# Performance work log

Hardware: AMD Instinct MI355X
Metric: run time of the kernel (lower is better)

The kernel has to match this reference:

```python
import jax, jax.numpy as jnp
import numpy as np

IOU_EPS = 1e-6  # eps from RotatedIoULoss init
LOSS_WEIGHT = 1.0


def cross2(a, b):
    return a[..., 0] * b[..., 1] - a[..., 1] * b[..., 0]


def box2corners(box):
    # box: (n,5) = (x, y, w, h, angle) -> corners (n,4,2), counter-clockwise
    x, y, w, h, a = (box[:, i] for i in range(5))
    tx = jnp.array([0.5, -0.5, -0.5, 0.5], dtype=box.dtype)
    ty = jnp.array([0.5, 0.5, -0.5, -0.5], dtype=box.dtype)
    cx = tx[None, :] * w[:, None]  # (n,4) local x
    cy = ty[None, :] * h[:, None]  # (n,4) local y
    cos, sin = jnp.cos(a)[:, None], jnp.sin(a)[:, None]
    rx = cx * cos - cy * sin + x[:, None]
    ry = cx * sin + cy * cos + y[:, None]
    return jnp.stack([rx, ry], axis=-1)


def box_intersection(c1, c2):
    # pairwise (aligned) edge-edge intersections: (n,4,4,2) points, (n,4,4) valid mask
    p1 = c1[:, :, None, :]                             # (n,4,1,2) edge starts of box1
    d1 = (jnp.roll(c1, -1, axis=1) - c1)[:, :, None, :]
    p2 = c2[:, None, :, :]                             # (n,1,4,2) edge starts of box2
    d2 = (jnp.roll(c2, -1, axis=1) - c2)[:, None, :, :]
    den = cross2(d1, d2)                               # (n,4,4)
    dp = p2 - p1
    safe = jnp.where(den == 0, 1.0, den)
    t = cross2(dp, d2) / safe
    u = cross2(dp, d1) / safe
    mask = (den != 0) & (t > 0) & (t < 1) & (u > 0) & (u < 1)
    pts = p1 + t[..., None] * d1
    return pts, mask


def box1_in_box2(c1, c2):
    # which corners of box1 lie strictly inside box2 (projection test, as in mmcv)
    a = c2[:, 0:1, :]
    b = c2[:, 1:2, :]
    d = c2[:, 3:4, :]
    ab, ad, am = b - a, d - a, c1 - a                  # (n,4,2)
    pab = jnp.sum(am * ab, -1)
    nab = jnp.sum(ab * ab, -1)
    pad = jnp.sum(am * ad, -1)
    nad = jnp.sum(ad * ad, -1)
    return (pab > 0) & (pab < nab) & (pad > 0) & (pad < nad)


def oriented_box_intersection_area(c1, c2):
    # convex intersection polygon area via vertex gathering + angular sort + shoelace
    inter_pts, inter_mask = box_intersection(c1, c2)
    m1 = box1_in_box2(c1, c2)                          # (n,4)
    m2 = box1_in_box2(c2, c1)                          # (n,4)
    n = c1.shape[0]
    verts = jnp.concatenate([c1, c2, inter_pts.reshape(n, 16, 2)], axis=1)  # (n,24,2)
    mask = jnp.concatenate([m1, m2, inter_mask.reshape(n, 16)], axis=1)     # (n,24)
    num = jnp.sum(mask, axis=1)                        # (n,) valid vertex count
    maskf = mask.astype(verts.dtype)[..., None]
    center = jnp.sum(verts * maskf, axis=1) / jnp.maximum(num, 1)[:, None].astype(verts.dtype)
    rel = verts - center[:, None, :]
    ang = jnp.arctan2(rel[..., 1], rel[..., 0])
    ang = jnp.where(mask, ang, 1e6)                    # invalid vertices sort last
    order = jnp.argsort(ang, axis=1)
    sv = jnp.take_along_axis(verts, order[..., None], axis=1)  # sorted CCW
    sm = jnp.take_along_axis(mask, order, axis=1)
    first = sv[:, 0:1, :]
    poly = jnp.where(sm[..., None], sv, first)         # pad with first vertex -> closed polygon
    nxt = jnp.roll(poly, -1, axis=1)
    area = 0.5 * jnp.abs(jnp.sum(cross2(poly, nxt), axis=1))
    return jnp.where(num >= 3, area, 0.0)


def diff_iou_rotated_2d(pred, target):
    c1 = box2corners(pred)
    c2 = box2corners(target)
    inter = oriented_box_intersection_area(c1, c2)
    a1 = pred[:, 2] * pred[:, 3]
    a2 = target[:, 2] * target[:, 3]
    return inter / (a1 + a2 - inter)


def setup_inputs() -> dict:
    key = jax.random.key(0)
    n = 1_000_000
    k1, k2, k3, k4, k5, k6 = jax.random.split(key, 6)
    xy = jax.random.uniform(k1, (n, 2), dtype=jnp.float32) * 512.0
    wh = jax.random.uniform(k2, (n, 2), dtype=jnp.float32) * 40.0 + 4.0
    ang = jax.random.uniform(k3, (n,), dtype=jnp.float32) * np.pi - np.pi / 2
    pred = jnp.concatenate([xy, wh, ang[:, None]], axis=1)
    # targets = perturbed preds, so boxes mostly overlap (realistic assigned pairs)
    dxy = jax.random.normal(k4, (n, 2), dtype=jnp.float32) * 2.0
    noise = jax.random.normal(k5, (n, 3), dtype=jnp.float32)
    twh = jnp.maximum(wh * (1.0 + 0.1 * noise[:, :2]), 1.0)
    target = jnp.concatenate([xy + dxy, twh, (ang + 0.1 * noise[:, 2])[:, None]], axis=1)
    weight = jax.random.uniform(k6, (n,), dtype=jnp.float32)
    return {"pred": pred, "target": target, "weight": weight}


def reference(pred, target, weight):
    ious = jnp.maximum(diff_iou_rotated_2d(pred, target), IOU_EPS)  # clamp(min=eps)
    loss = -jnp.log(ious)                                           # mode='log'
    loss = loss * weight                                            # weighted_loss
    return LOSS_WEIGHT * jnp.mean(loss)                             # reduction='mean'
```

## Files before the change

kernel.cpp:

```cpp
#include <hip/hip_runtime.h>
#include <math.h>


__device__ __forceinline__ float riou_one(float pw, float ph, float pa,
                                          float ox, float oy,
                                          float qw, float qh, float qa,
                                          float w)
{
    float ca = __cosf(pa), sa = __sinf(pa);
    float cb = __cosf(qa), sb = __sinf(qa);

    const float tx[4] = {0.5f, -0.5f, -0.5f, 0.5f};
    const float ty[4] = {0.5f, 0.5f, -0.5f, -0.5f};

    float c1x[4], c1y[4], c2x[4], c2y[4];
    #pragma unroll
    for (int i = 0; i < 4; i++) {
        float cx = tx[i] * pw, cy = ty[i] * ph;
        c1x[i] = cx * ca - cy * sa;
        c1y[i] = cx * sa + cy * ca;
        float dx = tx[i] * qw, dy = ty[i] * qh;
        c2x[i] = dx * cb - dy * sb + ox;
        c2y[i] = dx * sb + dy * cb + oy;
    }
    float e1x[4], e1y[4], e2x[4], e2y[4];
    #pragma unroll
    for (int i = 0; i < 4; i++) {
        e1x[i] = c1x[(i + 1) & 3] - c1x[i];
        e1y[i] = c1y[(i + 1) & 3] - c1y[i];
        e2x[i] = c2x[(i + 1) & 3] - c2x[i];
        e2y[i] = c2y[(i + 1) & 3] - c2y[i];
    }

    float acc = 0.0f;
    #pragma unroll
    for (int s = 0; s < 2; s++) {
        const float* ax_ = s ? c2x : c1x;
        const float* ay_ = s ? c2y : c1y;
        const float* dx_ = s ? e2x : e1x;
        const float* dy_ = s ? e2y : e1y;
        const float* bx_ = s ? c1x : c2x;
        const float* by_ = s ? c1y : c2y;
        const float* fx_ = s ? e1x : e2x;
        const float* fy_ = s ? e1y : e2y;

        #pragma unroll
        for (int i = 0; i < 4; i++) {
            float ax = ax_[i], ay = ay_[i];
            float dx = dx_[i], dy = dy_[i];
            float t0 = 0.0f, t1 = 1.0f;
            bool dead = false;
            #pragma unroll
            for (int j = 0; j < 4; j++) {
                float g = fx_[j] * dy - fy_[j] * dx;
                float f = fx_[j] * (ay - by_[j]) - fy_[j] * (ax - bx_[j]);
                float t = -f * __builtin_amdgcn_rcpf(g);
                t0 = fmaxf(t0, (g > 0.0f) ? t : 0.0f);
                t1 = fminf(t1, (g < 0.0f) ? t : 1.0f);
                dead = dead || ((g == 0.0f) && (f < 0.0f));
            }
            bool valid = (t1 > t0) && !dead;
            float sx = ax + t0 * dx, sy = ay + t0 * dy;
            float ex = ax + t1 * dx, ey = ay + t1 * dy;
            float c = sx * ey - sy * ex;
            acc += valid ? c : 0.0f;
        }
    }

    float inter = fmaxf(0.5f * acc, 0.0f);
    float a1 = pw * ph;
    float a2 = qw * qh;
    float iou = inter * __builtin_amdgcn_rcpf(a1 + a2 - inter);
    iou = fmaxf(iou, 1e-6f);
    return -__logf(iou) * w;
}

__global__ void __launch_bounds__(256)
riou_loss_kernel(const float* __restrict__ pred,
                 const float* __restrict__ target,
                 const float* __restrict__ weight,
                 float* __restrict__ out,
                 int n, float inv_n)
{
    int t = blockIdx.x * blockDim.x + threadIdx.x;
    int base = t * 4;
    float loss = 0.0f;

    if (base < n) {
        float pp[20], qq[20], ww[4];
        if (base + 4 <= n) {
            const float4* P4 = (const float4*)(pred   + (size_t)base * 5);
            const float4* Q4 = (const float4*)(target + (size_t)base * 5);
            #pragma unroll
            for (int i = 0; i < 5; i++) {
                float4 p = P4[i];
                pp[4 * i + 0] = p.x; pp[4 * i + 1] = p.y;
                pp[4 * i + 2] = p.z; pp[4 * i + 3] = p.w;
                float4 q = Q4[i];
                qq[4 * i + 0] = q.x; qq[4 * i + 1] = q.y;
                qq[4 * i + 2] = q.z; qq[4 * i + 3] = q.w;
            }
            float4 w4 = ((const float4*)weight)[t];
            ww[0] = w4.x; ww[1] = w4.y; ww[2] = w4.z; ww[3] = w4.w;
        } else {
            #pragma unroll
            for (int k = 0; k < 4; k++) {
                int b = base + k; b = (b < n) ? b : (n - 1);
                #pragma unroll
                for (int j = 0; j < 5; j++) {
                    pp[5 * k + j] = pred[(size_t)b * 5 + j];
                    qq[5 * k + j] = target[(size_t)b * 5 + j];
                }
                ww[k] = (base + k < n) ? weight[b] : 0.0f;
            }
        }

        bool vec = (base + 4 <= n);
        #pragma unroll
        for (int k = 0; k < 4; k++) {
            float px = pp[5 * k + 0], py = pp[5 * k + 1];
            float pw = pp[5 * k + 2], ph = pp[5 * k + 3], pa = pp[5 * k + 4];
            float qx = qq[5 * k + 0], qy = qq[5 * k + 1];
            float qw = qq[5 * k + 2], qh = qq[5 * k + 3], qa = qq[5 * k + 4];
            float w  = (vec || base + k < n) ? ww[k] : 0.0f;
            loss += riou_one(pw, ph, pa, qx - px, qy - py, qw, qh, qa, w);
        }
    }

    #pragma unroll
    for (int off = 32; off > 0; off >>= 1)
        loss += __shfl_down(loss, off, 64);

    __shared__ float ssum[4];
    int wave = threadIdx.x >> 6;
    int lane = threadIdx.x & 63;
    if (lane == 0) ssum[wave] = loss;
    __syncthreads();
    if (threadIdx.x == 0) {
        float s = ssum[0] + ssum[1] + ssum[2] + ssum[3];
        atomicAdd(out, s * inv_n);
    }
}

extern "C" void kernel_launch(void* const* d_in, const int* in_sizes, int n_in,
                              void* d_out, int out_size, void* d_ws, size_t ws_size,
                              hipStream_t stream) {
    const float* pred   = (const float*)d_in[0];
    const float* target = (const float*)d_in[1];
    const float* weight = (const float*)d_in[2];
    float* out = (float*)d_out;

    int n = in_sizes[0] / 5;

    hipMemsetAsync(out, 0, sizeof(float), stream);

    int block = 256;
    int threads_needed = (n + 3) / 4;
    int grid = (threads_needed + block - 1) / block;
    riou_loss_kernel<<<grid, block, 0, stream>>>(pred, target, weight, out,
                                                 n, 1.0f / (float)n);
}
```

Baseline: 98.51 us.

## Clip each box's edges in the other box's local frame as axis-aligned slabs

```diff
diff --git a/kernel.cpp b/kernel.cpp
--- a/kernel.cpp
+++ b/kernel.cpp
@@ -2,75 +2,86 @@
 #include <math.h>
 
 
-__device__ __forceinline__ float riou_one(float pw, float ph, float pa,
-                                          float ox, float oy,
-                                          float qw, float qh, float qa,
+__device__ __forceinline__ float rcpf(float x) { return __builtin_amdgcn_rcpf(x); }
+
+template <bool TRACK>
+__device__ __forceinline__ void clip_edge(float u0, float v0, float dx, float dy,
+                                          float rx, float ry, float hw, float hh,
+                                          float& S, float& Dx, float& Dy)
+{
+    float ta = (-hw - u0) * rx;
+    float tb = ( hw - u0) * rx;
+    float tc = (-hh - v0) * ry;
+    float td = ( hh - v0) * ry;
+    float tumin = fminf(ta, tb), tumax = fmaxf(ta, tb);
+    float tvmin = fminf(tc, td), tvmax = fmaxf(tc, td);
+    float t0 = fmaxf(fmaxf(tumin, tvmin), 0.0f);
+    float t1 = fminf(fminf(tumax, tvmax), 1.0f);
+    bool valid = t1 > t0;
+    float sx = fmaf(t0, dx, u0), sy = fmaf(t0, dy, v0);
+    float ex = fmaf(t1, dx, u0), ey = fmaf(t1, dy, v0);
+    float c = sx * ey - sy * ex;
+    S += valid ? c : 0.0f;
+    if (TRACK) {
+        Dx += valid ? (ex - sx) : 0.0f;
+        Dy += valid ? (ey - sy) : 0.0f;
+    }
+}
+
+template <bool TRACK>
+__device__ __forceinline__ float clip_quad(float Ux, float Uy, float Vx, float Vy,
+                                           float cx, float cy, float hw, float hh,
+                                           float& Dx, float& Dy)
+{
+    float d0x = -2.0f * Ux, d0y = -2.0f * Uy;
+    float d1x = -2.0f * Vx, d1y = -2.0f * Vy;
+    float r0x = rcpf(d0x), r0y = rcpf(d0y);
+    float r1x = rcpf(d1x), r1y = rcpf(d1y);
+
+    float sxv = Ux + Vx, syv = Uy + Vy;
+    float dxv = Ux - Vx, dyv = Uy - Vy;
+
+    float S = 0.0f;
+    clip_edge<TRACK>( sxv + cx,  syv + cy,  d0x,  d0y,  r0x,  r0y, hw, hh, S, Dx, Dy);
+    clip_edge<TRACK>(-dxv + cx, -dyv + cy,  d1x,  d1y,  r1x,  r1y, hw, hh, S, Dx, Dy);
+    clip_edge<TRACK>(-sxv + cx, -syv + cy, -d0x, -d0y, -r0x, -r0y, hw, hh, S, Dx, Dy);
+    clip_edge<TRACK>( dxv + cx,  dyv + cy, -d1x, -d1y, -r1x, -r1y, hw, hh, S, Dx, Dy);
+    return S;
+}
+
+__device__ __forceinline__ float riou_one(float px, float py, float pw, float ph, float pa,
+                                          float qx, float qy, float qw, float qh, float qa,
                                           float w)
 {
+    float hw1 = 0.5f * pw, hh1 = 0.5f * ph;
+    float hw2 = 0.5f * qw, hh2 = 0.5f * qh;
+
     float ca = __cosf(pa), sa = __sinf(pa);
-    float cb = __cosf(qa), sb = __sinf(qa);
+    float delta = pa - qa;
+    float cr = __cosf(delta), sr = __sinf(delta);
 
-    const float tx[4] = {0.5f, -0.5f, -0.5f, 0.5f};
-    const float ty[4] = {0.5f, 0.5f, -0.5f, -0.5f};
+    float ox = qx - px, oy = qy - py;
+    float cPx =  ca * ox + sa * oy;
+    float cPy = -sa * ox + ca * oy;
+    float cQx = -(cr * cPx - sr * cPy);
+    float cQy = -(sr * cPx + cr * cPy);
 
-    float c1x[4], c1y[4], c2x[4], c2y[4];
-    #pragma unroll
-    for (int i = 0; i < 4; i++) {
-        float cx = tx[i] * pw, cy = ty[i] * ph;
-        c1x[i] = cx * ca - cy * sa;
-        c1y[i] = cx * sa + cy * ca;
-        float dx = tx[i] * qw, dy = ty[i] * qh;
-        c2x[i] = dx * cb - dy * sb + ox;
-        c2y[i] = dx * sb + dy * cb + oy;
-    }
-    float e1x[4], e1y[4], e2x[4], e2y[4];
-    #pragma unroll
-    for (int i = 0; i < 4; i++) {
-        e1x[i] = c1x[(i + 1) & 3] - c1x[i];
-        e1y[i] = c1y[(i + 1) & 3] - c1y[i];
-        e2x[i] = c2x[(i + 1) & 3] - c2x[i];
-        e2y[i] = c2y[(i + 1) & 3] - c2y[i];
-    }
+    float dum0 = 0.0f, dum1 = 0.0f;
+    float SA = clip_quad<false>(cr * hw1, sr * hw1, -sr * hh1, cr * hh1,
+                                cQx, cQy, hw2, hh2, dum0, dum1);
 
-    float acc = 0.0f;
-    #pragma unroll
-    for (int s = 0; s < 2; s++) {
-        const float* ax_ = s ? c2x : c1x;
-        const float* ay_ = s ? c2y : c1y;
-        const float* dx_ = s ? e2x : e1x;
-        const float* dy_ = s ? e2y : e1y;
-        const float* bx_ = s ? c1x : c2x;
-        const float* by_ = s ? c1y : c2y;
-        const float* fx_ = s ? e1x : e2x;
-        const float* fy_ = s ? e1y : e2y;
+    float Dx = 0.0f, Dy = 0.0f;
+    float SB = clip_quad<true>(cr * hw2, -sr * hw2, sr * hh2, cr * hh2,
+                               cPx, cPy, hw1, hh1, Dx, Dy);
 
-        #pragma unroll
-        for (int i = 0; i < 4; i++) {
-            float ax = ax_[i], ay = ay_[i];
-            float dx = dx_[i], dy = dy_[i];
-            float t0 = 0.0f, t1 = 1.0f;
-            bool dead = false;
-            #pragma unroll
-            for (int j = 0; j < 4; j++) {
-                float g = fx_[j] * dy - fy_[j] * dx;
-                float f = fx_[j] * (ay - by_[j]) - fy_[j] * (ax - bx_[j]);
-                float t = -f * __builtin_amdgcn_rcpf(g);
-                t0 = fmaxf(t0, (g > 0.0f) ? t : 0.0f);
-                t1 = fminf(t1, (g < 0.0f) ? t : 1.0f);
-                dead = dead || ((g == 0.0f) && (f < 0.0f));
-            }
-            bool valid = (t1 > t0) && !dead;
-            float sx = ax + t0 * dx, sy = ay + t0 * dy;
-            float ex = ax + t1 * dx, ey = ay + t1 * dy;
-            float c = sx * ey - sy * ex;
-            acc += valid ? c : 0.0f;
-        }
-    }
+    float RDx = cr * Dx - sr * Dy;
+    float RDy = sr * Dx + cr * Dy;
+    float corr = cQx * RDy - cQy * RDx;
 
-    float inter = fmaxf(0.5f * acc, 0.0f);
+    float inter = fmaxf(0.5f * (SA + SB + corr), 0.0f);
     float a1 = pw * ph;
     float a2 = qw * qh;
-    float iou = inter * __builtin_amdgcn_rcpf(a1 + a2 - inter);
+    float iou = inter * rcpf(a1 + a2 - inter);
     iou = fmaxf(iou, 1e-6f);
     return -__logf(iou) * w;
 }
@@ -115,15 +126,13 @@
             }
         }
 
-        bool vec = (base + 4 <= n);
         #pragma unroll
         for (int k = 0; k < 4; k++) {
-            float px = pp[5 * k + 0], py = pp[5 * k + 1];
-            float pw = pp[5 * k + 2], ph = pp[5 * k + 3], pa = pp[5 * k + 4];
-            float qx = qq[5 * k + 0], qy = qq[5 * k + 1];
-            float qw = qq[5 * k + 2], qh = qq[5 * k + 3], qa = qq[5 * k + 4];
-            float w  = (vec || base + k < n) ? ww[k] : 0.0f;
-            loss += riou_one(pw, ph, pa, qx - px, qy - py, qw, qh, qa, w);
+            loss += riou_one(pp[5 * k + 0], pp[5 * k + 1], pp[5 * k + 2],
+                             pp[5 * k + 3], pp[5 * k + 4],
+                             qq[5 * k + 0], qq[5 * k + 1], qq[5 * k + 2],
+                             qq[5 * k + 3], qq[5 * k + 4],
+                             ww[k]);
         }
     }
 
```

Result: faster. 93.72 us (-4.9%).
